# Optimization experiments

Hardware: AMD Instinct MI355X
Metric: run time of the kernel (lower is better)

## Reference

```python
import jax, jax.numpy as jnp
import numpy as np

B, D, K = 65536, 128, 8
BOUND = 3.0
MIN_BIN_W = 1e-3   # min_bin_width
MIN_BIN_H = 1e-3   # min_bin_height
MIN_DERIV = 1e-3   # min_derivative
EPS = 1e-6


def setup_inputs() -> dict:
    key = jax.random.key(0)
    k1, k2, k3, k4 = jax.random.split(key, 4)
    return {
        "x": jax.random.normal(k1, (B, D), jnp.float32) * 1.5,
        "unnormalized_widths": jax.random.normal(k2, (D, K), jnp.float32),
        "unnormalized_heights": jax.random.normal(k3, (D, K), jnp.float32),
        "unnormalized_derivatives": jax.random.normal(k4, (D, K - 1), jnp.float32),
    }


def _calculate_knots(lengths, lower, upper):
    # lengths: [D, K] summing to ~1 -> scaled lengths and knot positions [D, K+1]
    knots = jnp.cumsum(lengths, axis=-1)
    knots = jnp.pad(knots, ((0, 0), (1, 0)))
    knots = (upper - lower) * knots + lower
    knots = knots.at[..., 0].set(lower)
    knots = knots.at[..., -1].set(upper)
    return knots[..., 1:] - knots[..., :-1], knots


def _select_bins(p, idx):
    # p: [D, Kp] per-dim tables, idx: [B, D] bin indices -> [B, D]
    i = jnp.clip(idx, 0, p.shape[-1] - 1)
    return p[jnp.arange(p.shape[0])[None, :], i]


def _spline_forward(x, uw, uh, ud):
    w = jax.nn.softmax(uw, axis=-1)
    h = jax.nn.softmax(uh, axis=-1)
    d = jax.nn.softplus(ud)

    num_bins = w.shape[-1]
    widths = MIN_BIN_W + (1.0 - MIN_BIN_W * num_bins) * w
    heights = MIN_BIN_H + (1.0 - MIN_BIN_H * num_bins) * h
    derivs = jnp.pad(MIN_DERIV + d, ((0, 0), (1, 1)), constant_values=1.0 - MIN_DERIV)  # [D, K+1]

    widths, cumwidths = _calculate_knots(widths, -BOUND, BOUND)
    heights, cumheights = _calculate_knots(heights, -BOUND, BOUND)

    inside = (x >= -BOUND) & (x <= BOUND)
    xc = jnp.clip(x, -BOUND, BOUND)  # keep tail values finite; masked out below

    # searchsorted: which bin each input falls into   [B, D]
    bin_idx = jnp.sum(xc[..., None] >= (cumwidths + EPS)[None, :, :], axis=-1) - 1

    iw = _select_bins(widths, bin_idx)
    icw = _select_bins(cumwidths, bin_idx)
    ich = _select_bins(cumheights, bin_idx)
    idelta = _select_bins(heights / widths, bin_idx)
    id0 = _select_bins(derivs, bin_idx)
    id1 = _select_bins(derivs[..., 1:], bin_idx)
    ih = _select_bins(heights, bin_idx)

    # rational quadratic spline (forward)
    theta = (xc - icw) / iw
    t1m = theta * (1.0 - theta)
    numerator = ih * (idelta * theta ** 2 + id0 * t1m)
    denominator = idelta + (id0 + id1 - 2.0 * idelta) * t1m
    out = ich + numerator / denominator
    dnum = idelta ** 2 * (id1 * theta ** 2 + 2.0 * idelta * t1m + id0 * (1.0 - theta) ** 2)
    lad = jnp.log(dnum) - 2.0 * jnp.log(denominator)

    u = jnp.where(inside, out, x)          # identity outside tail bound
    lad = jnp.where(inside, lad, 0.0)
    return u, lad


def reference(x, unnormalized_widths, unnormalized_heights, unnormalized_derivatives):
    u, lad = _spline_forward(x, unnormalized_widths, unnormalized_heights, unnormalized_derivatives)
    log_detJ = jnp.sum(lad, axis=1)
    return u, log_detJ
```

## Files before the change

### kernel.cpp

```cpp
#include <hip/hip_runtime.h>
#include <math.h>

namespace {
constexpr int D = 128;
constexpr int K = 8;
constexpr float BOUND = 3.0f;
constexpr float EPS = 1e-6f;
constexpr float MIN_BIN_W = 1e-3f;
constexpr float MIN_BIN_H = 1e-3f;
constexpr float MIN_DERIV = 1e-3f;
constexpr float LN2 = 0.6931471805599453f;
constexpr int REC = 8;
constexpr int S = K * REC + 4;
constexpr int WPB = 8;
constexpr int PPW = 4;
}

__device__ __forceinline__ float spline_elem(float xv, const float* __restrict__ row,
                                             const float* kn, float* __restrict__ outp) {
    const bool inside = (xv >= -BOUND) & (xv <= BOUND);
    const float xc = fminf(fmaxf(xv, -BOUND), BOUND);
    int idx = 0;
    #pragma unroll
    for (int j = 0; j < 7; ++j) idx += (xc >= kn[j]) ? 1 : 0;
    const float4 ra = *(const float4*)(row + idx * REC);
    const float4 rb = *(const float4*)(row + idx * REC + 4);
    const float theta = (xc - ra.x) * ra.y;
    const float omt   = 1.f - theta;
    const float t1m   = theta * omt;
    const float th2   = theta * theta;
    const float num   = rb.y * (ra.w * th2 + ra.z * t1m);
    const float den   = ra.w + rb.w * t1m;
    const float rd    = __builtin_amdgcn_rcpf(den);
    const float outv  = fmaf(num, rd, rb.x);
    const float dnum  = ra.w * ra.w * (rb.z * th2 + 2.f * ra.w * t1m + ra.z * omt * omt);
    const float lad   = __log2f(dnum * rd * rd);
    *outp = inside ? outv : xv;
    return inside ? lad : 0.f;
}

__global__ __launch_bounds__(512, 8) void spline_fwd(
    const float* __restrict__ x,
    const float* __restrict__ uw,
    const float* __restrict__ uh,
    const float* __restrict__ ud,
    float* __restrict__ out_u,
    float* __restrict__ out_ld,
    int nrows)
{
    __shared__ __align__(16) float s_tab[D * S];

    const int tid = threadIdx.x;
    if (tid < D) {
        const int d = tid;
        float wv[K], hv[K], cw[K + 1], ch[K + 1], der[K + 1];

        {
            const float* p = uw + d * K;
            float m = p[0];
            #pragma unroll
            for (int j = 1; j < K; ++j) m = fmaxf(m, p[j]);
            float s = 0.f;
            #pragma unroll
            for (int j = 0; j < K; ++j) { wv[j] = __expf(p[j] - m); s += wv[j]; }
            const float inv = __builtin_amdgcn_rcpf(s) * (1.f - MIN_BIN_W * K);
            #pragma unroll
            for (int j = 0; j < K; ++j) wv[j] = MIN_BIN_W + wv[j] * inv;
        }
        {
            const float* p = uh + d * K;
            float m = p[0];
            #pragma unroll
            for (int j = 1; j < K; ++j) m = fmaxf(m, p[j]);
            float s = 0.f;
            #pragma unroll
            for (int j = 0; j < K; ++j) { hv[j] = __expf(p[j] - m); s += hv[j]; }
            const float inv = __builtin_amdgcn_rcpf(s) * (1.f - MIN_BIN_H * K);
            #pragma unroll
            for (int j = 0; j < K; ++j) hv[j] = MIN_BIN_H + hv[j] * inv;
        }
        cw[0] = -BOUND; ch[0] = -BOUND;
        float cs_w = 0.f, cs_h = 0.f;
        #pragma unroll
        for (int j = 0; j < K; ++j) {
            cs_w += wv[j]; cw[j + 1] = 2.f * BOUND * cs_w - BOUND;
            cs_h += hv[j]; ch[j + 1] = 2.f * BOUND * cs_h - BOUND;
        }
        cw[K] = BOUND; ch[K] = BOUND;

        der[0] = 1.f - MIN_DERIV;
        der[K] = 1.f - MIN_DERIV;
        {
            const float* p = ud + d * (K - 1);
            #pragma unroll
            for (int j = 1; j < K; ++j) {
                const float v = p[j - 1];
                const float sp = log1pf(__expf(-fabsf(v))) + fmaxf(v, 0.f);
                der[j] = MIN_DERIV + sp;
            }
        }

        float* row = s_tab + ((d & 3) * 32 + (d >> 2)) * S;
        #pragma unroll
        for (int j = 0; j < K; ++j) {
            const float w  = cw[j + 1] - cw[j];
            const float h  = ch[j + 1] - ch[j];
            const float iw = 1.f / w;
            const float dl = h * iw;
            row[j * REC + 0] = cw[j];
            row[j * REC + 1] = iw;
            row[j * REC + 2] = der[j];
            row[j * REC + 3] = dl;
            row[j * REC + 4] = ch[j];
            row[j * REC + 5] = h;
            row[j * REC + 6] = der[j + 1];
            row[j * REC + 7] = der[j] + der[j + 1] - 2.f * dl;
        }
    }
    __syncthreads();

    const int wave = tid >> 6;
    const int lane = tid & 63;
    const int l32  = lane & 31;
    const int half = lane >> 5;

    const float* rowp0 = s_tab + (0 * 32 + l32) * S;
    const float* rowp1 = s_tab + (1 * 32 + l32) * S;
    const float* rowp2 = s_tab + (2 * 32 + l32) * S;
    const float* rowp3 = s_tab + (3 * 32 + l32) * S;

    float kn[28];
    #pragma unroll
    for (int j = 0; j < 7; ++j) {
        kn[j]      = rowp0[(j + 1) * REC] + EPS;
        kn[7 + j]  = rowp1[(j + 1) * REC] + EPS;
        kn[14 + j] = rowp2[(j + 1) * REC] + EPS;
        kn[21 + j] = rowp3[(j + 1) * REC] + EPS;
    }

    const int p0 = (blockIdx.x * WPB + wave) * PPW;
    const int lo4 = lane << 2;

    float4 xcur = *(const float4*)(x + (size_t)(p0 * 2) * D + lo4);
    #pragma unroll
    for (int c = 0; c < PPW; ++c) {
        const int p = p0 + c;
        float4 xnext;
        if (c + 1 < PPW)
            xnext = *(const float4*)(x + (size_t)((p + 1) * 2) * D + lo4);

        float4 u;
        float la;
        la  = spline_elem(xcur.x, rowp0, kn +  0, &u.x);
        la += spline_elem(xcur.y, rowp1, kn +  7, &u.y);
        la += spline_elem(xcur.z, rowp2, kn + 14, &u.z);
        la += spline_elem(xcur.w, rowp3, kn + 21, &u.w);

        *(float4*)(out_u + (size_t)(p * 2) * D + lo4) = u;

        la += __shfl_xor(la, 1);
        la += __shfl_xor(la, 2);
        la += __shfl_xor(la, 4);
        la += __shfl_xor(la, 8);
        la += __shfl_xor(la, 16);
        if (l32 == 0) out_ld[p * 2 + half] = la * LN2;

        xcur = xnext;
    }
}

extern "C" void kernel_launch(void* const* d_in, const int* in_sizes, int n_in,
                              void* d_out, int out_size, void* d_ws, size_t ws_size,
                              hipStream_t stream) {
    const float* x  = (const float*)d_in[0];
    const float* uw = (const float*)d_in[1];
    const float* uh = (const float*)d_in[2];
    const float* ud = (const float*)d_in[3];
    const int nrows = in_sizes[0] / D;
    float* out_u  = (float*)d_out;
    float* out_ld = (float*)d_out + (size_t)nrows * D;
    const int npairs = nrows / 2;
    const int nblocks = (npairs + WPB * PPW - 1) / (WPB * PPW);
    spline_fwd<<<nblocks, 512, 0, stream>>>(x, uw, uh, ud, out_u, out_ld, nrows);
}
```

Baseline: 119.4 us.

## Restructure spline table into SoA float4 arrays and process one row per wave

Stores the per-bin coefficient table as two structure-of-arrays float4 tables indexed by bin and dimension slot, replacing the padded per-dimension row layout. Each wave now handles 8 full rows with float2 loads per lane, not 4 row pairs with float4 loads. The row sum moves from a 32-lane to a 64-lane shuffle reduction, and the register footprint drops to 14 knots. It also swaps rcp for exact division in the softmax setup and lowers the launch-bounds occupancy hint. The goal is fewer LDS bank conflicts on the gathered table reads, at the cost of narrower global accesses and dropping the x prefetch.

```diff
diff --git a/kernel.cpp b/kernel.cpp
--- a/kernel.cpp
+++ b/kernel.cpp
@@ -10,21 +10,21 @@
 constexpr float MIN_BIN_H = 1e-3f;
 constexpr float MIN_DERIV = 1e-3f;
 constexpr float LN2 = 0.6931471805599453f;
-constexpr int REC = 8;
-constexpr int S = K * REC + 4;
 constexpr int WPB = 8;
-constexpr int PPW = 4;
+constexpr int RPW = 8;
 }
 
-__device__ __forceinline__ float spline_elem(float xv, const float* __restrict__ row,
-                                             const float* kn, float* __restrict__ outp) {
+__device__ __forceinline__ float spline_elem(float xv, int slot, const float* kn,
+                                             const float4* __restrict__ A,
+                                             const float4* __restrict__ B,
+                                             float* __restrict__ outp) {
     const bool inside = (xv >= -BOUND) & (xv <= BOUND);
     const float xc = fminf(fmaxf(xv, -BOUND), BOUND);
     int idx = 0;
     #pragma unroll
     for (int j = 0; j < 7; ++j) idx += (xc >= kn[j]) ? 1 : 0;
-    const float4 ra = *(const float4*)(row + idx * REC);
-    const float4 rb = *(const float4*)(row + idx * REC + 4);
+    const float4 ra = A[idx * D + slot];
+    const float4 rb = B[idx * D + slot];
     const float theta = (xc - ra.x) * ra.y;
     const float omt   = 1.f - theta;
     const float t1m   = theta * omt;
@@ -39,7 +39,7 @@
     return inside ? lad : 0.f;
 }
 
-__global__ __launch_bounds__(512, 8) void spline_fwd(
+__global__ __launch_bounds__(512, 6) void spline_fwd(
     const float* __restrict__ x,
     const float* __restrict__ uw,
     const float* __restrict__ uh,
@@ -48,7 +48,8 @@
     float* __restrict__ out_ld,
     int nrows)
 {
-    __shared__ __align__(16) float s_tab[D * S];
+    __shared__ __align__(16) float4 s_A[K * D];
+    __shared__ __align__(16) float4 s_B[K * D];
 
     const int tid = threadIdx.x;
     if (tid < D) {
@@ -63,7 +64,7 @@
             float s = 0.f;
             #pragma unroll
             for (int j = 0; j < K; ++j) { wv[j] = __expf(p[j] - m); s += wv[j]; }
-            const float inv = __builtin_amdgcn_rcpf(s) * (1.f - MIN_BIN_W * K);
+            const float inv = (1.f - MIN_BIN_W * K) / s;
             #pragma unroll
             for (int j = 0; j < K; ++j) wv[j] = MIN_BIN_W + wv[j] * inv;
         }
@@ -75,7 +76,7 @@
             float s = 0.f;
             #pragma unroll
             for (int j = 0; j < K; ++j) { hv[j] = __expf(p[j] - m); s += hv[j]; }
-            const float inv = __builtin_amdgcn_rcpf(s) * (1.f - MIN_BIN_H * K);
+            const float inv = (1.f - MIN_BIN_H * K) / s;
             #pragma unroll
             for (int j = 0; j < K; ++j) hv[j] = MIN_BIN_H + hv[j] * inv;
         }
@@ -100,72 +101,53 @@
             }
         }
 
-        float* row = s_tab + ((d & 3) * 32 + (d >> 2)) * S;
+        const int slot = (d & 1) * 64 + (d >> 1);
         #pragma unroll
         for (int j = 0; j < K; ++j) {
             const float w  = cw[j + 1] - cw[j];
             const float h  = ch[j + 1] - ch[j];
             const float iw = 1.f / w;
             const float dl = h * iw;
-            row[j * REC + 0] = cw[j];
-            row[j * REC + 1] = iw;
-            row[j * REC + 2] = der[j];
-            row[j * REC + 3] = dl;
-            row[j * REC + 4] = ch[j];
-            row[j * REC + 5] = h;
-            row[j * REC + 6] = der[j + 1];
-            row[j * REC + 7] = der[j] + der[j + 1] - 2.f * dl;
+            s_A[j * D + slot] = make_float4(cw[j], iw, der[j], dl);
+            s_B[j * D + slot] = make_float4(ch[j], h, der[j + 1],
+                                            der[j] + der[j + 1] - 2.f * dl);
         }
     }
     __syncthreads();
 
     const int wave = tid >> 6;
     const int lane = tid & 63;
-    const int l32  = lane & 31;
-    const int half = lane >> 5;
+    const int slot0 = lane;
+    const int slot1 = 64 + lane;
 
-    const float* rowp0 = s_tab + (0 * 32 + l32) * S;
-    const float* rowp1 = s_tab + (1 * 32 + l32) * S;
-    const float* rowp2 = s_tab + (2 * 32 + l32) * S;
-    const float* rowp3 = s_tab + (3 * 32 + l32) * S;
-
-    float kn[28];
+    float kn0[7], kn1[7];
     #pragma unroll
     for (int j = 0; j < 7; ++j) {
-        kn[j]      = rowp0[(j + 1) * REC] + EPS;
-        kn[7 + j]  = rowp1[(j + 1) * REC] + EPS;
-        kn[14 + j] = rowp2[(j + 1) * REC] + EPS;
-        kn[21 + j] = rowp3[(j + 1) * REC] + EPS;
+        kn0[j] = s_A[(j + 1) * D + slot0].x + EPS;
+        kn1[j] = s_A[(j + 1) * D + slot1].x + EPS;
     }
 
-    const int p0 = (blockIdx.x * WPB + wave) * PPW;
-    const int lo4 = lane << 2;
+    const int r0 = (blockIdx.x * WPB + wave) * RPW;
+    const int lo2 = lane * 2;
 
-    float4 xcur = *(const float4*)(x + (size_t)(p0 * 2) * D + lo4);
     #pragma unroll
-    for (int c = 0; c < PPW; ++c) {
-        const int p = p0 + c;
-        float4 xnext;
-        if (c + 1 < PPW)
-            xnext = *(const float4*)(x + (size_t)((p + 1) * 2) * D + lo4);
+    for (int i = 0; i < RPW; ++i) {
+        const int r = r0 + i;
+        if (r < nrows) {
+            const float2 xv = *(const float2*)(x + (size_t)r * D + lo2);
+            float u0, u1;
+            float la = spline_elem(xv.x, slot0, kn0, s_A, s_B, &u0)
+                     + spline_elem(xv.y, slot1, kn1, s_A, s_B, &u1);
+            *(float2*)(out_u + (size_t)r * D + lo2) = make_float2(u0, u1);
 
-        float4 u;
-        float la;
-        la  = spline_elem(xcur.x, rowp0, kn +  0, &u.x);
-        la += spline_elem(xcur.y, rowp1, kn +  7, &u.y);
-        la += spline_elem(xcur.z, rowp2, kn + 14, &u.z);
-        la += spline_elem(xcur.w, rowp3, kn + 21, &u.w);
-
-        *(float4*)(out_u + (size_t)(p * 2) * D + lo4) = u;
-
-        la += __shfl_xor(la, 1);
-        la += __shfl_xor(la, 2);
-        la += __shfl_xor(la, 4);
-        la += __shfl_xor(la, 8);
-        la += __shfl_xor(la, 16);
-        if (l32 == 0) out_ld[p * 2 + half] = la * LN2;
-
-        xcur = xnext;
+            la += __shfl_xor(la, 1);
+            la += __shfl_xor(la, 2);
+            la += __shfl_xor(la, 4);
+            la += __shfl_xor(la, 8);
+            la += __shfl_xor(la, 16);
+            la += __shfl_xor(la, 32);
+            if (lane == 0) out_ld[r] = la * LN2;
+        }
     }
 }
 
@@ -179,7 +161,6 @@
     const int nrows = in_sizes[0] / D;
     float* out_u  = (float*)d_out;
     float* out_ld = (float*)d_out + (size_t)nrows * D;
-    const int npairs = nrows / 2;
-    const int nblocks = (npairs + WPB * PPW - 1) / (WPB * PPW);
+    const int nblocks = (nrows + WPB * RPW - 1) / (WPB * RPW);
     spline_fwd<<<nblocks, 512, 0, stream>>>(x, uw, uh, ud, out_u, out_ld, nrows);
 }
```

Measured after the change: 100.1 us. 1.19x faster.
